# Optimization experiments

Hardware: AMD Instinct MI355X
Metric: run time of the kernel (lower is better)

The kernel has to match this reference:

```python
import jax, jax.numpy as jnp
import numpy as np

N_NODES = 100000
N_EDGES = 1600000
IN_FEATS = 128
H_FEATS = 128


def setup_inputs() -> dict:
    key = jax.random.key(0)
    ks = jax.random.split(key, 8)
    in_feat = jax.random.normal(ks[0], (N_NODES, IN_FEATS), dtype=jnp.float32)
    src = jax.random.randint(ks[1], (N_EDGES,), 0, N_NODES, dtype=jnp.int32)
    dst = jax.random.randint(ks[2], (N_EDGES,), 0, N_NODES, dtype=jnp.int32)
    # GraphConv weights are (in, out); xavier-ish scaling
    W1 = jax.random.normal(ks[3], (IN_FEATS, 2 * H_FEATS), dtype=jnp.float32) * (2.0 / (IN_FEATS + 2 * H_FEATS)) ** 0.5
    b1 = jnp.zeros((2 * H_FEATS,), dtype=jnp.float32)
    W2 = jax.random.normal(ks[4], (2 * H_FEATS, H_FEATS), dtype=jnp.float32) * (2.0 / (3 * H_FEATS)) ** 0.5
    b2 = jnp.zeros((H_FEATS,), dtype=jnp.float32)
    fc1_w = jax.random.normal(ks[5], (H_FEATS, H_FEATS), dtype=jnp.float32) * (1.0 / H_FEATS) ** 0.5
    fc2_w = jax.random.normal(ks[6], (H_FEATS, H_FEATS), dtype=jnp.float32) * (1.0 / H_FEATS) ** 0.5
    return {"in_feat": in_feat, "src": src, "dst": dst, "W1": W1, "b1": b1,
            "W2": W2, "b2": b2, "fc1_w": fc1_w, "fc2_w": fc2_w}


def _degrees(src, dst):
    ones = jnp.ones((src.shape[0],), dtype=jnp.float32)
    out_deg = jax.ops.segment_sum(ones, src, num_segments=N_NODES)
    in_deg = jax.ops.segment_sum(ones, dst, num_segments=N_NODES)
    # DGL norm='both': clamp degree to >= 1
    return jnp.clip(out_deg, 1.0), jnp.clip(in_deg, 1.0)


def _graph_conv(x, W, b, src, dst, out_norm, in_norm):
    # norm='both': scale src feats by D_out^{-1/2}, sum-aggregate, scale by D_in^{-1/2}
    # DGL applies W first when in_feats > out_feats (saves memory/flops)
    if W.shape[0] > W.shape[1]:
        x = x @ W
        x = x * out_norm[:, None]
        agg = jax.ops.segment_sum(x[src], dst, num_segments=N_NODES)
        rst = agg * in_norm[:, None]
    else:
        x = x * out_norm[:, None]
        agg = jax.ops.segment_sum(x[src], dst, num_segments=N_NODES)
        rst = (agg * in_norm[:, None]) @ W
    return rst + b


def reference(in_feat, src, dst, W1, b1, W2, b2, fc1_w, fc2_w):
    out_deg, in_deg = _degrees(src, dst)
    out_norm = jax.lax.rsqrt(out_deg)
    in_norm = jax.lax.rsqrt(in_deg)
    h = _graph_conv(in_feat, W1, b1, src, dst, out_norm, in_norm)
    h = jax.nn.relu(h)
    h = _graph_conv(h, W2, b2, src, dst, out_norm, in_norm)
    h = jax.nn.relu(h)
    feat1 = h @ fc1_w.T  # nn.Linear, bias=False
    feat2 = h @ fc2_w.T
    return (h, feat1, feat2)
```

## Files before the change

kernel.cpp:

```cpp
#include <hip/hip_runtime.h>

#define N_NODES 100000
#define N_EDGES 1600000
#define P_PARTS 8
#define S_SLICES 32
#define NP 12500
#define ES 50000

typedef __attribute__((ext_vector_type(8))) short short8;
typedef __attribute__((ext_vector_type(4))) float f32x4;

__device__ inline float bf2f(unsigned short h) {
    union { unsigned int u; float f; } v; v.u = ((unsigned int)h) << 16; return v.f;
}
__device__ inline unsigned short f2bf(float f) {
    union { unsigned int u; float f; } v; v.f = f;
    unsigned int u = v.u;
    return (unsigned short)((u + 0x7fffu + ((u >> 16) & 1u)) >> 16);
}

__global__ __launch_bounds__(256) void hist_part_kernel(
    const int* __restrict__ src, const int* __restrict__ dst,
    int* __restrict__ part_src, int* __restrict__ part_dst) {
    __shared__ int hs[NP];
    __shared__ int hd[NP];
    int tid = threadIdx.x;
    int p = blockIdx.x & (P_PARTS - 1), s = blockIdx.x >> 3;
    for (int j = tid; j < NP; j += 256) { hs[j] = 0; hd[j] = 0; }
    __syncthreads();
    int lo = p * NP;
    const int4* s4 = (const int4*)(src + s * ES);
    const int4* d4 = (const int4*)(dst + s * ES);
    for (int i = tid; i < ES / 4; i += 256) {
        int4 sv = s4[i];
        int4 dv = d4[i];
        int a;
        a = sv.x - lo; if ((unsigned)a < NP) atomicAdd(&hs[a], 1);
        a = sv.y - lo; if ((unsigned)a < NP) atomicAdd(&hs[a], 1);
        a = sv.z - lo; if ((unsigned)a < NP) atomicAdd(&hs[a], 1);
        a = sv.w - lo; if ((unsigned)a < NP) atomicAdd(&hs[a], 1);
        a = dv.x - lo; if ((unsigned)a < NP) atomicAdd(&hd[a], 1);
        a = dv.y - lo; if ((unsigned)a < NP) atomicAdd(&hd[a], 1);
        a = dv.z - lo; if ((unsigned)a < NP) atomicAdd(&hd[a], 1);
        a = dv.w - lo; if ((unsigned)a < NP) atomicAdd(&hd[a], 1);
    }
    __syncthreads();
    int* ps = part_src + (size_t)(p * S_SLICES + s) * NP;
    int* pd = part_dst + (size_t)(p * S_SLICES + s) * NP;
    for (int j = tid; j < NP; j += 256) { ps[j] = hs[j]; pd[j] = hd[j]; }
}

__global__ void reduce_prefix_norm_kernel(const int* __restrict__ part_src,
                                          int* __restrict__ part_dst,
                                          int* __restrict__ deg_in,
                                          float* __restrict__ out_norm,
                                          float* __restrict__ in_norm) {
    int n = blockIdx.x * blockDim.x + threadIdx.x;
    if (n >= N_NODES) return;
    int p = n / NP, j = n - p * NP;
    size_t base = (size_t)p * S_SLICES * NP + j;
    int so = 0;
    #pragma unroll
    for (int s = 0; s < S_SLICES; s++) so += part_src[base + (size_t)s * NP];
    int run = 0;
    #pragma unroll
    for (int s = 0; s < S_SLICES; s++) {
        int c = part_dst[base + (size_t)s * NP];
        part_dst[base + (size_t)s * NP] = run;
        run += c;
    }
    deg_in[n] = run;
    out_norm[n] = rsqrtf((float)(so < 1 ? 1 : so));
    in_norm[n]  = rsqrtf((float)(run < 1 ? 1 : run));
}

__global__ void scan_kernel(const int* __restrict__ deg, int* __restrict__ row_ptr) {
    __shared__ int sums[1024];
    int t = threadIdx.x;
    int s = 0;
    if (t < 1000) {
        const int4* d4 = (const int4*)(deg + t * 100);
        #pragma unroll
        for (int i = 0; i < 25; i++) { int4 v = d4[i]; s += v.x + v.y + v.z + v.w; }
    }
    sums[t] = s;
    __syncthreads();
    for (int st = 1; st < 1024; st <<= 1) {
        int v = (t >= st) ? sums[t - st] : 0;
        __syncthreads();
        sums[t] += v;
        __syncthreads();
    }
    if (t < 1000) {
        int base = (t == 0) ? 0 : sums[t - 1];
        for (int i = 0; i < 100; i++) { row_ptr[t * 100 + i] = base; base += deg[t * 100 + i]; }
    }
    if (t == 1023) row_ptr[N_NODES] = sums[1023];
}

__global__ __launch_bounds__(256) void fill_part_kernel(
    const int* __restrict__ src, const int* __restrict__ dst,
    const int* __restrict__ row_ptr, const int* __restrict__ part_dst,
    int* __restrict__ csr_src) {
    __shared__ int cnt[NP];
    int tid = threadIdx.x;
    int p = blockIdx.x & (P_PARTS - 1), s = blockIdx.x >> 3;
    for (int j = tid; j < NP; j += 256) cnt[j] = 0;
    __syncthreads();
    int lo = p * NP;
    const int* pd = part_dst + (size_t)(p * S_SLICES + s) * NP;
    const int4* s4 = (const int4*)(src + s * ES);
    const int4* d4 = (const int4*)(dst + s * ES);
    for (int i = tid; i < ES / 4; i += 256) {
        int4 sv = s4[i];
        int4 dv = d4[i];
        int a;
        a = dv.x - lo;
        if ((unsigned)a < NP) { int r = atomicAdd(&cnt[a], 1); csr_src[row_ptr[lo + a] + pd[a] + r] = sv.x; }
        a = dv.y - lo;
        if ((unsigned)a < NP) { int r = atomicAdd(&cnt[a], 1); csr_src[row_ptr[lo + a] + pd[a] + r] = sv.y; }
        a = dv.z - lo;
        if ((unsigned)a < NP) { int r = atomicAdd(&cnt[a], 1); csr_src[row_ptr[lo + a] + pd[a] + r] = sv.z; }
        a = dv.w - lo;
        if ((unsigned)a < NP) { int r = atomicAdd(&cnt[a], 1); csr_src[row_ptr[lo + a] + pd[a] + r] = sv.w; }
    }
}

__global__ void tconv_kernel(const float* __restrict__ in, unsigned short* __restrict__ out,
                             int NN, int KK) {
    int idx = blockIdx.x * blockDim.x + threadIdx.x;
    if (idx >= NN * KK) return;
    int n = idx / KK, k = idx % KK;
    out[idx] = f2bf(in[(size_t)k * NN + n]);
}
__global__ void conv_kernel(const float* __restrict__ in, unsigned short* __restrict__ out,
                            int total) {
    int idx = blockIdx.x * blockDim.x + threadIdx.x;
    if (idx < total) out[idx] = f2bf(in[idx]);
}

__global__ void prescale_kernel(const float4* __restrict__ in, const float* __restrict__ out_norm,
                                ushort4* __restrict__ out) {
    int idx = blockIdx.x * blockDim.x + threadIdx.x;
    if (idx >= N_NODES * 32) return;
    float sc = out_norm[idx >> 5];
    float4 v = in[idx];
    ushort4 o;
    o.x = f2bf(v.x * sc); o.y = f2bf(v.y * sc); o.z = f2bf(v.z * sc); o.w = f2bf(v.w * sc);
    out[idx] = o;
}

template<int EPI>
__global__ __launch_bounds__(256) void aggregate_bf(
    const ushort4* __restrict__ x, const int* __restrict__ row_ptr,
    const int* __restrict__ csr_src, const float* __restrict__ in_norm,
    const float* __restrict__ b2, float4* __restrict__ outF,
    ushort4* __restrict__ outB) {
    int wave = threadIdx.x >> 6, lane = threadIdx.x & 63;
    int n = blockIdx.x * 4 + wave;
    if (n >= N_NODES) return;
    int half = lane >> 5, cl = lane & 31;
    int s0 = row_ptr[n], s1 = row_ptr[n + 1];
    float ax = 0, ay = 0, az = 0, aw = 0;
    float bx = 0, by = 0, bz = 0, bw = 0;
    int i = s0 + half;
    for (; i + 6 < s1; i += 8) {
        int sA = csr_src[i],     sB = csr_src[i + 2];
        int sC = csr_src[i + 4], sD = csr_src[i + 6];
        ushort4 va = x[(size_t)sA * 32 + cl];
        ushort4 vb = x[(size_t)sB * 32 + cl];
        ushort4 vc = x[(size_t)sC * 32 + cl];
        ushort4 vd = x[(size_t)sD * 32 + cl];
        ax += bf2f(va.x); ay += bf2f(va.y); az += bf2f(va.z); aw += bf2f(va.w);
        bx += bf2f(vb.x); by += bf2f(vb.y); bz += bf2f(vb.z); bw += bf2f(vb.w);
        ax += bf2f(vc.x); ay += bf2f(vc.y); az += bf2f(vc.z); aw += bf2f(vc.w);
        bx += bf2f(vd.x); by += bf2f(vd.y); bz += bf2f(vd.z); bw += bf2f(vd.w);
    }
    for (; i < s1; i += 2) {
        ushort4 va = x[(size_t)csr_src[i] * 32 + cl];
        ax += bf2f(va.x); ay += bf2f(va.y); az += bf2f(va.z); aw += bf2f(va.w);
    }
    ax += bx; ay += by; az += bz; aw += bw;
    ax += __shfl_xor(ax, 32);
    ay += __shfl_xor(ay, 32);
    az += __shfl_xor(az, 32);
    aw += __shfl_xor(aw, 32);
    float inn = in_norm[n];
    if (EPI == 0) {
        if (half == 0) {
            ushort4 o;
            o.x = f2bf(ax * inn); o.y = f2bf(ay * inn);
            o.z = f2bf(az * inn); o.w = f2bf(aw * inn);
            outB[(size_t)n * 32 + cl] = o;
        }
    } else {
        float4 bv = ((const float4*)b2)[cl];
        float vx = fmaxf(fmaf(ax, inn, bv.x), 0.f);
        float vy = fmaxf(fmaf(ay, inn, bv.y), 0.f);
        float vz = fmaxf(fmaf(az, inn, bv.z), 0.f);
        float vw = fmaxf(fmaf(aw, inn, bv.w), 0.f);
        if (half == 0) {
            outF[(size_t)n * 32 + cl] = make_float4(vx, vy, vz, vw);
        } else {
            ushort4 o;
            o.x = f2bf(vx); o.y = f2bf(vy); o.z = f2bf(vz); o.w = f2bf(vw);
            outB[(size_t)n * 32 + cl] = o;
        }
    }
}

template<int K, int EPI>
__global__ __launch_bounds__(256) void gemm_mfma(
    const unsigned short* __restrict__ A, const unsigned short* __restrict__ Bt,
    const float* __restrict__ aux, void* __restrict__ Cv, int ldc, int M) {
    constexpr int CH = K / 8;
    __shared__ short blds[128 * K];
    int tid = threadIdx.x;
    int bn = blockIdx.x * 128;
    int bm = blockIdx.y * 128;
    {
        const short8* g = (const short8*)Bt;
        short8* l = (short8*)blds;
        for (int id = tid; id < 128 * CH; id += 256) {
            int col = id / CH, kc = id % CH;
            l[col * CH + (kc ^ (col & (CH - 1)))] = g[(size_t)(bn + col) * CH + kc];
        }
    }
    __syncthreads();
    int wm = tid >> 6, lane = tid & 63;
    int lr = lane & 15, kq = lane >> 4;
    int r0 = bm + wm * 32 + lr;
    int r1 = r0 + 16;
    const short8* A8 = (const short8*)A;
    size_t a0row = (size_t)(r0 < M ? r0 : 0) * CH;
    size_t a1row = (size_t)(r1 < M ? r1 : 0) * CH;
    const short8* l8 = (const short8*)blds;

    f32x4 acc[2][8];
    #pragma unroll
    for (int m = 0; m < 2; m++)
        #pragma unroll
        for (int j = 0; j < 8; j++) acc[m][j] = (f32x4)0.f;

    short8 a0 = A8[a0row + kq];
    short8 a1 = A8[a1row + kq];
    for (int kc2 = 0; kc2 < K / 32; kc2++) {
        int kc = kc2 * 4 + kq;
        short8 n0, n1;
        if (kc2 + 1 < K / 32) {
            n0 = A8[a0row + kc + 4];
            n1 = A8[a1row + kc + 4];
        }
        #pragma unroll
        for (int nj = 0; nj < 8; nj++) {
            int col = nj * 16 + lr;
            short8 b = l8[col * CH + (kc ^ (col & (CH - 1)))];
            acc[0][nj] = __builtin_amdgcn_mfma_f32_16x16x32_bf16(a0, b, acc[0][nj], 0, 0, 0);
            acc[1][nj] = __builtin_amdgcn_mfma_f32_16x16x32_bf16(a1, b, acc[1][nj], 0, 0, 0);
        }
        a0 = n0; a1 = n1;
    }

    #pragma unroll
    for (int mi = 0; mi < 2; mi++) {
        #pragma unroll
        for (int i = 0; i < 4; i++) {
            int gr = bm + wm * 32 + mi * 16 + kq * 4 + i;
            if (gr >= M) continue;
            float sc = (EPI == 2) ? aux[gr] : 0.f;
            #pragma unroll
            for (int nj = 0; nj < 8; nj++) {
                int col = bn + nj * 16 + lr;
                float v = acc[mi][nj][i];
                if (EPI == 0)
                    ((float*)Cv)[(size_t)gr * ldc + col] = v;
                else if (EPI == 1)
                    ((unsigned short*)Cv)[(size_t)gr * ldc + col] = f2bf(fmaxf(v + aux[col], 0.f));
                else
                    ((unsigned short*)Cv)[(size_t)gr * ldc + col] = f2bf(v * sc);
            }
        }
    }
}

extern "C" void kernel_launch(void* const* d_in, const int* in_sizes, int n_in,
                              void* d_out, int out_size, void* d_ws, size_t ws_size,
                              hipStream_t stream) {
    const float* in_feat = (const float*)d_in[0];
    const int*   src     = (const int*)d_in[1];
    const int*   dst     = (const int*)d_in[2];
    const float* W1      = (const float*)d_in[3];
    const float* b1      = (const float*)d_in[4];
    const float* W2      = (const float*)d_in[5];
    const float* b2      = (const float*)d_in[6];
    const float* fc1_w   = (const float*)d_in[7];
    const float* fc2_w   = (const float*)d_in[8];

    float* out = (float*)d_out;
    float* h_out = out;
    float* feat1 = out + (size_t)12800000;
    float* feat2 = out + (size_t)25600000;
    unsigned short* xs_bf   = (unsigned short*)out;
    unsigned short* agg1_bf = (unsigned short*)(out + 6400000);
    unsigned short* h1_bf   = (unsigned short*)(out + 12800000);
    unsigned short* x2_bf   = (unsigned short*)(out + 25600000);

    int* part_dst = (int*)d_ws;
    int* part_src = part_dst + P_PARTS * S_SLICES * NP;
    int* csr_src  = part_src;
    int* deg_in   = part_src + P_PARTS * S_SLICES * NP;
    int* row_ptr  = deg_in + 100000;
    float* out_norm = (float*)(row_ptr + 100004);
    float* in_norm  = out_norm + 100000;
    unsigned short* Wt1  = (unsigned short*)(in_norm + 100000);
    unsigned short* Wt2  = Wt1 + 32768;
    unsigned short* fc1b = Wt2 + 32768;
    unsigned short* fc2b = fc1b + 16384;
    unsigned short* h_bf = fc2b + 16384;

    hist_part_kernel<<<P_PARTS * S_SLICES, 256, 0, stream>>>(src, dst, part_src, part_dst);
    reduce_prefix_norm_kernel<<<(N_NODES + 255) / 256, 256, 0, stream>>>(
        part_src, part_dst, deg_in, out_norm, in_norm);
    scan_kernel<<<1, 1024, 0, stream>>>(deg_in, row_ptr);
    fill_part_kernel<<<P_PARTS * S_SLICES, 256, 0, stream>>>(src, dst, row_ptr, part_dst, csr_src);

    tconv_kernel<<<128, 256, 0, stream>>>(W1, Wt1, 256, 128);
    tconv_kernel<<<128, 256, 0, stream>>>(W2, Wt2, 128, 256);
    conv_kernel<<<64, 256, 0, stream>>>(fc1_w, fc1b, 16384);
    conv_kernel<<<64, 256, 0, stream>>>(fc2_w, fc2b, 16384);

    prescale_kernel<<<12500, 256, 0, stream>>>((const float4*)in_feat, out_norm, (ushort4*)xs_bf);

    aggregate_bf<0><<<25000, 256, 0, stream>>>((const ushort4*)xs_bf, row_ptr, csr_src,
                                               in_norm, nullptr, nullptr, (ushort4*)agg1_bf);

    gemm_mfma<128, 1><<<dim3(2, 782), 256, 0, stream>>>(agg1_bf, Wt1, b1, h1_bf, 256, N_NODES);
    gemm_mfma<256, 2><<<dim3(1, 782), 256, 0, stream>>>(h1_bf, Wt2, out_norm, x2_bf, 128, N_NODES);

    aggregate_bf<1><<<25000, 256, 0, stream>>>((const ushort4*)x2_bf, row_ptr, csr_src,
                                               in_norm, b2, (float4*)h_out, (ushort4*)h_bf);

    gemm_mfma<128, 0><<<dim3(1, 782), 256, 0, stream>>>(h_bf, fc1b, nullptr, feat1, 128, N_NODES);
    gemm_mfma<128, 0><<<dim3(1, 782), 256, 0, stream>>>(h_bf, fc2b, nullptr, feat2, 128, N_NODES);
}
```

Measured before the change: 405.2 us.

## Widen aggregation loads, merge weight prep and fuse fc1/fc2 GEMMs

Result: no change. 400.2 us (-1.2%).

```diff
diff --git a/kernel.cpp b/kernel.cpp
--- a/kernel.cpp
+++ b/kernel.cpp
@@ -6,8 +6,10 @@
 #define S_SLICES 32
 #define NP 12500
 #define ES 50000
+#define FEAT2_OFF 12800000
 
 typedef __attribute__((ext_vector_type(8))) short short8;
+typedef __attribute__((ext_vector_type(8))) unsigned short ushort8v;
 typedef __attribute__((ext_vector_type(4))) float f32x4;
 
 __device__ inline float bf2f(unsigned short h) {
@@ -126,17 +128,22 @@
     }
 }
 
-__global__ void tconv_kernel(const float* __restrict__ in, unsigned short* __restrict__ out,
-                             int NN, int KK) {
+__global__ void prep_weights_kernel(const float* __restrict__ W1, const float* __restrict__ W2,
+                                    const float* __restrict__ fc1, const float* __restrict__ fc2,
+                                    unsigned short* __restrict__ Wt1, unsigned short* __restrict__ Wt2,
+                                    unsigned short* __restrict__ fcb) {
     int idx = blockIdx.x * blockDim.x + threadIdx.x;
-    if (idx >= NN * KK) return;
-    int n = idx / KK, k = idx % KK;
-    out[idx] = f2bf(in[(size_t)k * NN + n]);
-}
-__global__ void conv_kernel(const float* __restrict__ in, unsigned short* __restrict__ out,
-                            int total) {
-    int idx = blockIdx.x * blockDim.x + threadIdx.x;
-    if (idx < total) out[idx] = f2bf(in[idx]);
+    if (idx < 32768) {
+        int n = idx >> 7, k = idx & 127;
+        Wt1[idx] = f2bf(W1[k * 256 + n]);
+    } else if (idx < 65536) {
+        int t = idx - 32768;
+        int n = t >> 8, k = t & 255;
+        Wt2[t] = f2bf(W2[k * 128 + n]);
+    } else if (idx < 98304) {
+        int t = idx - 65536;
+        fcb[t] = f2bf(t < 16384 ? fc1[t] : fc2[t - 16384]);
+    }
 }
 
 __global__ void prescale_kernel(const float4* __restrict__ in, const float* __restrict__ out_norm,
@@ -152,76 +159,90 @@
 
 template<int EPI>
 __global__ __launch_bounds__(256) void aggregate_bf(
-    const ushort4* __restrict__ x, const int* __restrict__ row_ptr,
+    const unsigned short* __restrict__ x, const int* __restrict__ row_ptr,
     const int* __restrict__ csr_src, const float* __restrict__ in_norm,
     const float* __restrict__ b2, float4* __restrict__ outF,
-    ushort4* __restrict__ outB) {
+    unsigned short* __restrict__ outB) {
     int wave = threadIdx.x >> 6, lane = threadIdx.x & 63;
     int n = blockIdx.x * 4 + wave;
     if (n >= N_NODES) return;
-    int half = lane >> 5, cl = lane & 31;
+    int q = lane >> 4, ql = lane & 15;
     int s0 = row_ptr[n], s1 = row_ptr[n + 1];
-    float ax = 0, ay = 0, az = 0, aw = 0;
-    float bx = 0, by = 0, bz = 0, bw = 0;
-    int i = s0 + half;
-    for (; i + 6 < s1; i += 8) {
-        int sA = csr_src[i],     sB = csr_src[i + 2];
-        int sC = csr_src[i + 4], sD = csr_src[i + 6];
-        ushort4 va = x[(size_t)sA * 32 + cl];
-        ushort4 vb = x[(size_t)sB * 32 + cl];
-        ushort4 vc = x[(size_t)sC * 32 + cl];
-        ushort4 vd = x[(size_t)sD * 32 + cl];
-        ax += bf2f(va.x); ay += bf2f(va.y); az += bf2f(va.z); aw += bf2f(va.w);
-        bx += bf2f(vb.x); by += bf2f(vb.y); bz += bf2f(vb.z); bw += bf2f(vb.w);
-        ax += bf2f(vc.x); ay += bf2f(vc.y); az += bf2f(vc.z); aw += bf2f(vc.w);
-        bx += bf2f(vd.x); by += bf2f(vd.y); bz += bf2f(vd.z); bw += bf2f(vd.w);
-    }
-    for (; i < s1; i += 2) {
-        ushort4 va = x[(size_t)csr_src[i] * 32 + cl];
-        ax += bf2f(va.x); ay += bf2f(va.y); az += bf2f(va.z); aw += bf2f(va.w);
-    }
-    ax += bx; ay += by; az += bz; aw += bw;
-    ax += __shfl_xor(ax, 32);
-    ay += __shfl_xor(ay, 32);
-    az += __shfl_xor(az, 32);
-    aw += __shfl_xor(aw, 32);
+    const ushort8v* xf = (const ushort8v*)x;
+    float a0[8], a1[8];
+    #pragma unroll
+    for (int j = 0; j < 8; j++) { a0[j] = 0.f; a1[j] = 0.f; }
+    int i = s0 + q;
+    for (; i + 12 < s1; i += 16) {
+        int sA = csr_src[i],     sB = csr_src[i + 4];
+        int sC = csr_src[i + 8], sD = csr_src[i + 12];
+        ushort8v va = xf[(size_t)sA * 16 + ql];
+        ushort8v vb = xf[(size_t)sB * 16 + ql];
+        ushort8v vc = xf[(size_t)sC * 16 + ql];
+        ushort8v vd = xf[(size_t)sD * 16 + ql];
+        #pragma unroll
+        for (int j = 0; j < 8; j++) a0[j] += bf2f(va[j]) + bf2f(vc[j]);
+        #pragma unroll
+        for (int j = 0; j < 8; j++) a1[j] += bf2f(vb[j]) + bf2f(vd[j]);
+    }
+    for (; i < s1; i += 4) {
+        ushort8v va = xf[(size_t)csr_src[i] * 16 + ql];
+        #pragma unroll
+        for (int j = 0; j < 8; j++) a0[j] += bf2f(va[j]);
+    }
+    #pragma unroll
+    for (int j = 0; j < 8; j++) {
+        float v = a0[j] + a1[j];
+        v += __shfl_xor(v, 16);
+        v += __shfl_xor(v, 32);
+        a0[j] = v;
+    }
     float inn = in_norm[n];
     if (EPI == 0) {
-        if (half == 0) {
-            ushort4 o;
-            o.x = f2bf(ax * inn); o.y = f2bf(ay * inn);
-            o.z = f2bf(az * inn); o.w = f2bf(aw * inn);
-            outB[(size_t)n * 32 + cl] = o;
+        if (q == 0) {
+            ushort8v o;
+            #pragma unroll
+            for (int j = 0; j < 8; j++) o[j] = f2bf(a0[j] * inn);
+            ((ushort8v*)outB)[(size_t)n * 16 + ql] = o;
         }
     } else {
-        float4 bv = ((const float4*)b2)[cl];
-        float vx = fmaxf(fmaf(ax, inn, bv.x), 0.f);
-        float vy = fmaxf(fmaf(ay, inn, bv.y), 0.f);
-        float vz = fmaxf(fmaf(az, inn, bv.z), 0.f);
-        float vw = fmaxf(fmaf(aw, inn, bv.w), 0.f);
-        if (half == 0) {
-            outF[(size_t)n * 32 + cl] = make_float4(vx, vy, vz, vw);
-        } else {
-            ushort4 o;
-            o.x = f2bf(vx); o.y = f2bf(vy); o.z = f2bf(vz); o.w = f2bf(vw);
-            outB[(size_t)n * 32 + cl] = o;
-        }
-    }
-}
-
-template<int K, int EPI>
+        const float4* b4 = (const float4*)b2;
+        float4 blo = b4[ql * 2], bhi = b4[ql * 2 + 1];
+        float v[8];
+        v[0] = fmaxf(fmaf(a0[0], inn, blo.x), 0.f);
+        v[1] = fmaxf(fmaf(a0[1], inn, blo.y), 0.f);
+        v[2] = fmaxf(fmaf(a0[2], inn, blo.z), 0.f);
+        v[3] = fmaxf(fmaf(a0[3], inn, blo.w), 0.f);
+        v[4] = fmaxf(fmaf(a0[4], inn, bhi.x), 0.f);
+        v[5] = fmaxf(fmaf(a0[5], inn, bhi.y), 0.f);
+        v[6] = fmaxf(fmaf(a0[6], inn, bhi.z), 0.f);
+        v[7] = fmaxf(fmaf(a0[7], inn, bhi.w), 0.f);
+        if (q == 0) {
+            ushort8v o;
+            #pragma unroll
+            for (int j = 0; j < 8; j++) o[j] = f2bf(v[j]);
+            ((ushort8v*)outB)[(size_t)n * 16 + ql] = o;
+        } else if (q == 1) {
+            outF[(size_t)n * 32 + ql * 2] = make_float4(v[0], v[1], v[2], v[3]);
+        } else if (q == 2) {
+            outF[(size_t)n * 32 + ql * 2 + 1] = make_float4(v[4], v[5], v[6], v[7]);
+        }
+    }
+}
+
+template<int K, int NF, int EPI>
 __global__ __launch_bounds__(256) void gemm_mfma(
     const unsigned short* __restrict__ A, const unsigned short* __restrict__ Bt,
     const float* __restrict__ aux, void* __restrict__ Cv, int ldc, int M) {
     constexpr int CH = K / 8;
-    __shared__ short blds[128 * K];
+    __shared__ short blds[NF * 16 * K];
     int tid = threadIdx.x;
-    int bn = blockIdx.x * 128;
+    int bn = blockIdx.x * (NF * 16);
     int bm = blockIdx.y * 128;
     {
         const short8* g = (const short8*)Bt;
         short8* l = (short8*)blds;
-        for (int id = tid; id < 128 * CH; id += 256) {
+        for (int id = tid; id < NF * 16 * CH; id += 256) {
             int col = id / CH, kc = id % CH;
             l[col * CH + (kc ^ (col & (CH - 1)))] = g[(size_t)(bn + col) * CH + kc];
         }
@@ -236,11 +257,11 @@
     size_t a1row = (size_t)(r1 < M ? r1 : 0) * CH;
     const short8* l8 = (const short8*)blds;
 
-    f32x4 acc[2][8];
+    f32x4 acc[2][NF];
     #pragma unroll
     for (int m = 0; m < 2; m++)
         #pragma unroll
-        for (int j = 0; j < 8; j++) acc[m][j] = (f32x4)0.f;
+        for (int j = 0; j < NF; j++) acc[m][j] = (f32x4)0.f;
 
     short8 a0 = A8[a0row + kq];
     short8 a1 = A8[a1row + kq];
@@ -252,7 +273,7 @@
             n1 = A8[a1row + kc + 4];
         }
         #pragma unroll
-        for (int nj = 0; nj < 8; nj++) {
+        for (int nj = 0; nj < NF; nj++) {
             int col = nj * 16 + lr;
             short8 b = l8[col * CH + (kc ^ (col & (CH - 1)))];
             acc[0][nj] = __builtin_amdgcn_mfma_f32_16x16x32_bf16(a0, b, acc[0][nj], 0, 0, 0);
@@ -269,15 +290,18 @@
             if (gr >= M) continue;
             float sc = (EPI == 2) ? aux[gr] : 0.f;
             #pragma unroll
-            for (int nj = 0; nj < 8; nj++) {
+            for (int nj = 0; nj < NF; nj++) {
                 int col = bn + nj * 16 + lr;
                 float v = acc[mi][nj][i];
-                if (EPI == 0)
-                    ((float*)Cv)[(size_t)gr * ldc + col] = v;
-                else if (EPI == 1)
+                if (EPI == 1)
                     ((unsigned short*)Cv)[(size_t)gr * ldc + col] = f2bf(fmaxf(v + aux[col], 0.f));
-                else
+                else if (EPI == 2)
                     ((unsigned short*)Cv)[(size_t)gr * ldc + col] = f2bf(v * sc);
+                else {
+                    float* dstp = (float*)Cv + (size_t)(col >= 128 ? FEAT2_OFF : 0)
+                                  + (size_t)gr * 128 + (col & 127);
+                    *dstp = v;
+                }
             }
         }
     }
@@ -299,7 +323,6 @@
     float* out = (float*)d_out;
     float* h_out = out;
     float* feat1 = out + (size_t)12800000;
-    float* feat2 = out + (size_t)25600000;
     unsigned short* xs_bf   = (unsigned short*)out;
     unsigned short* agg1_bf = (unsigned short*)(out + 6400000);
     unsigned short* h1_bf   = (unsigned short*)(out + 12800000);
@@ -312,11 +335,10 @@
     int* row_ptr  = deg_in + 100000;
     float* out_norm = (float*)(row_ptr + 100004);
     float* in_norm  = out_norm + 100000;
-    unsigned short* Wt1  = (unsigned short*)(in_norm + 100000);
-    unsigned short* Wt2  = Wt1 + 32768;
-    unsigned short* fc1b = Wt2 + 32768;
-    unsigned short* fc2b = fc1b + 16384;
-    unsigned short* h_bf = fc2b + 16384;
+    unsigned short* Wt1 = (unsigned short*)(in_norm + 100000);
+    unsigned short* Wt2 = Wt1 + 32768;
+    unsigned short* fcb = Wt2 + 32768;
+    unsigned short* h_bf = fcb + 32768;
 
     hist_part_kernel<<<P_PARTS * S_SLICES, 256, 0, stream>>>(src, dst, part_src, part_dst);
     reduce_prefix_norm_kernel<<<(N_NODES + 255) / 256, 256, 0, stream>>>(
@@ -324,22 +346,18 @@
     scan_kernel<<<1, 1024, 0, stream>>>(deg_in, row_ptr);
     fill_part_kernel<<<P_PARTS * S_SLICES, 256, 0, stream>>>(src, dst, row_ptr, part_dst, csr_src);
 
-    tconv_kernel<<<128, 256, 0, stream>>>(W1, Wt1, 256, 128);
-    tconv_kernel<<<128, 256, 0, stream>>>(W2, Wt2, 128, 256);
-    conv_kernel<<<64, 256, 0, stream>>>(fc1_w, fc1b, 16384);
-    conv_kernel<<<64, 256, 0, stream>>>(fc2_w, fc2b, 16384);
+    prep_weights_kernel<<<384, 256, 0, stream>>>(W1, W2, fc1_w, fc2_w, Wt1, Wt2, fcb);
 
     prescale_kernel<<<12500, 256, 0, stream>>>((const float4*)in_feat, out_norm, (ushort4*)xs_bf);
 
-    aggregate_bf<0><<<25000, 256, 0, stream>>>((const ushort4*)xs_bf, row_ptr, csr_src,
-                                               in_norm, nullptr, nullptr, (ushort4*)agg1_bf);
-
-    gemm_mfma<128, 1><<<dim3(2, 782), 256, 0, stream>>>(agg1_bf, Wt1, b1, h1_bf, 256, N_NODES);
-    gemm_mfma<256, 2><<<dim3(1, 782), 256, 0, stream>>>(h1_bf, Wt2, out_norm, x2_bf, 128, N_NODES);
-
-    aggregate_bf<1><<<25000, 256, 0, stream>>>((const ushort4*)x2_bf, row_ptr, csr_src,
-                                               in_norm, b2, (float4*)h_out, (ushort4*)h_bf);
-
-    gemm_mfma<128, 0><<<dim3(1, 782), 256, 0, stream>>>(h_bf, fc1b, nullptr, feat1, 128, N_NODES);
-    gemm_mfma<128, 0><<<dim3(1, 782), 256, 0, stream>>>(h_bf, fc2b, nullptr, feat2, 128, N_NODES);
-}
+    aggregate_bf<0><<<25000, 256, 0, stream>>>(xs_bf, row_ptr, csr_src,
+                                               in_norm, nullptr, nullptr, agg1_bf);
+
+    gemm_mfma<128, 16, 1><<<dim3(1, 782), 256, 0, stream>>>(agg1_bf, Wt1, b1, h1_bf, 256, N_NODES);
+    gemm_mfma<256, 8, 2><<<dim3(1, 782), 256, 0, stream>>>(h1_bf, Wt2, out_norm, x2_bf, 128, N_NODES);
+
+    aggregate_bf<1><<<25000, 256, 0, stream>>>(x2_bf, row_ptr, csr_src,
+                                               in_norm, b2, (float4*)h_out, h_bf);
+
+    gemm_mfma<128, 16, 3><<<dim3(1, 782), 256, 0, stream>>>(h_bf, fcb, nullptr, feat1, 128, N_NODES);
+}
```
